# Performance work log

Measured on AMD Instinct MI355X. Metric: run time of the kernel, lower is better.

## Reference

```python
import jax, jax.numpy as jnp
from jax import lax
import numpy as np

GAMMA = 0.25        # inv_temp
C_SCALE = 1.0       # spectral_scale
STRIDE = 8          # patch stride (== patch_size, non-overlapping)


def setup_inputs() -> dict:
    key = jax.random.key(0)
    ks = jax.random.split(key, 9)
    B, C, H = 1024, 3, 64
    D, NP, M, NH, R, P = 256, 64, 1024, 8, 32, 8
    return {
        "x": jax.random.normal(ks[0], (B, C, H, H), jnp.float32),
        "z": jax.random.normal(ks[1], (B, NP, D), jnp.float32),
        "encoder_weight": jax.random.normal(ks[2], (D, C, P, P), jnp.float32) * 0.05,
        "encoder_bias": jax.random.normal(ks[3], (D,), jnp.float32) * 0.05,
        "visible_bias": jax.random.normal(ks[4], (C, H, H), jnp.float32) * 0.05,
        "pos_bias": jax.random.normal(ks[5], (NP, D), jnp.float32) * 0.05,
        "memory_weight": jax.random.normal(ks[6], (D, M), jnp.float32) * 0.05,
        "W_Q": jax.random.normal(ks[7], (NH, R, D), jnp.float32) * 0.05,
        "W_K": jax.random.normal(ks[8], (NH, R, D), jnp.float32) * 0.05,
    }


def reference(x, z, encoder_weight, encoder_bias, visible_bias, pos_bias,
              memory_weight, W_Q, W_K):
    """E = 0.5||x||^2 + 0.5||z||^2 - Phi_coupling(x, z); returns (B,)."""
    B = x.shape[0]
    D = encoder_weight.shape[0]

    quad_x = 0.5 * jnp.sum(x * x, axis=(1, 2, 3))
    quad_z = 0.5 * jnp.sum(z * z, axis=(1, 2))

    # visible-bias coupling
    phi_vis = jnp.sum(visible_bias[None] * x, axis=(1, 2, 3))

    # conv encode: (B, D, gh, gw) -> (B, NP, D)
    enc = lax.conv_general_dilated(
        x, C_SCALE * encoder_weight, window_strides=(STRIDE, STRIDE),
        padding='VALID', dimension_numbers=('NCHW', 'OIHW', 'NCHW'))
    encoded = enc.reshape(B, D, -1).transpose(0, 2, 1)  # (B, NP, D)

    # enc_act = 'none' -> identity
    phi_enc = jnp.sum(encoded * z, axis=(1, 2))
    phi_bias = jnp.sum(z * encoder_bias, axis=(1, 2))
    phi_pos = jnp.sum(z * pos_bias[None], axis=(1, 2))

    # memory ReLU^2 term: (B, NP, M)
    mem_proj = jnp.einsum('bpd,dm->bpm', z, C_SCALE * memory_weight)
    phi_mem = jnp.sum(jnp.square(jax.nn.relu(mem_proj)), axis=(1, 2))

    # Hopfield attention logsumexp term
    Q = jnp.einsum('bpd,hrd->bhrp', z, C_SCALE * W_Q)  # (B, H, R, NP)
    K = jnp.einsum('bpd,hrd->bhrp', z, C_SCALE * W_K)
    A = jnp.einsum('bhdm,bhdn->bhmn', Q, K)            # (B, H, NP, NP)
    phi_att = jnp.sum(jax.scipy.special.logsumexp(GAMMA * A, axis=-1),
                      axis=(1, 2)) / GAMMA

    coupling = phi_vis + phi_enc + phi_bias + phi_pos + phi_mem + phi_att
    return quad_x + quad_z - coupling
```

## Files before the change

### kernel.cpp

```cpp
#include <hip/hip_runtime.h>
#include <hip/hip_bf16.h>

#define GAMMA 0.25f


typedef __attribute__((ext_vector_type(8))) short short8;
typedef __attribute__((ext_vector_type(4))) float f32x4;

__device__ __forceinline__ float dot4(float4 a, float4 b) {
  return fmaf(a.x, b.x, fmaf(a.y, b.y, fmaf(a.z, b.z, a.w * b.w)));
}

__device__ __forceinline__ void fma4(float4& a, float s, float4 w) {
  a.x = fmaf(s, w.x, a.x); a.y = fmaf(s, w.y, a.y);
  a.z = fmaf(s, w.z, a.z); a.w = fmaf(s, w.w, a.w);
}

__device__ __forceinline__ ushort f2bf(float f) {
  __hip_bfloat16 h = __float2bfloat16(f);
  return *reinterpret_cast<ushort*>(&h);
}

__device__ __forceinline__ float bf2f(ushort u) {
  union { unsigned int i; float f; } v;
  v.i = ((unsigned int)u) << 16;
  return v.f;
}

__device__ __forceinline__ void bar_lds() {
  asm volatile("s_waitcnt lgkmcnt(0)" ::: "memory");
  __builtin_amdgcn_s_barrier();
  asm volatile("" ::: "memory");
}

__device__ __forceinline__ float block_sum_256(float v, float* tmp) {
#pragma unroll
  for (int off = 32; off; off >>= 1) v += __shfl_down(v, off, 64);
  int w = threadIdx.x >> 6;
  if ((threadIdx.x & 63) == 0) tmp[w] = v;
  __syncthreads();
  return tmp[0] + tmp[1] + tmp[2] + tmp[3];
}

__global__ __launch_bounds__(256) void k_z_cvt2(const float* __restrict__ z,
                                                const float* __restrict__ eb,
                                                const float* __restrict__ pb,
                                                float* __restrict__ out,
                                                ushort* __restrict__ zb16) {
  __shared__ float tmp[4];
  int bid = blockIdx.x, b = bid >> 1, hz = bid & 1, t = threadIdx.x;
  const float4* zb = (const float4*)(z + (size_t)b * 16384);
  const float4* pb4 = (const float4*)pb;
  const float4* eb4 = (const float4*)eb;
  ushort4* z16o = (ushort4*)(zb16 + (size_t)b * 16384);
  float s = 0.f;
  const int i0 = hz * 2048;
  for (int i = i0 + t; i < i0 + 2048; i += 256) {
    float4 zv = zb[i];
    float4 pv = pb4[i];
    float4 ev = eb4[i & 63];
    float4 c;
    c.x = pv.x + ev.x; c.y = pv.y + ev.y; c.z = pv.z + ev.z; c.w = pv.w + ev.w;
    s += 0.5f * dot4(zv, zv) - dot4(zv, c);
    ushort4 o;
    o.x = f2bf(zv.x); o.y = f2bf(zv.y); o.z = f2bf(zv.z); o.w = f2bf(zv.w);
    z16o[i] = o;
  }
  float r = block_sum_256(s, tmp);
  if (t == 0) atomicAdd(out + b, r);
}

__global__ __launch_bounds__(256) void k_cvt_weights_v3(
    const float* __restrict__ wq, const float* __restrict__ wk,
    const float* __restrict__ ew, const float* __restrict__ mw,
    ushort* __restrict__ wqf, ushort* __restrict__ wkf,
    ushort* __restrict__ ewt, ushort* __restrict__ mtf) {
  int bid = blockIdx.x, t = threadIdx.x;
  ushort o[8];
  if (bid < 64) {
    const float* src = (bid < 32) ? wq : wk;
    ushort* dst = (bid < 32) ? wqf : wkf;
    int tid = (bid & 31) * 256 + t;
    int frag = tid >> 6, l = tid & 63;
    int h = frag >> 4, nt = (frag >> 3) & 1, ks = frag & 7;
    const float* s = src + ((size_t)h * 32 + nt * 16 + (l & 15)) * 256 +
                     ks * 32 + (l >> 4) * 8;
#pragma unroll
    for (int i = 0; i < 8; ++i) o[i] = f2bf(s[i]);
    *(ushort4*)(dst + (size_t)tid * 8) = *(ushort4*)&o[0];
    *(ushort4*)(dst + (size_t)tid * 8 + 4) = *(ushort4*)&o[4];
  } else if (bid < 88) {
    int tid = (bid - 64) * 256 + t;
    int frag = tid >> 6, l = tid & 63;
    int ks = frag / 12, ct = frag % 12;
    const float* s = ew + (size_t)(ks * 32 + (l >> 4) * 8) * 192 +
                     ct * 16 + (l & 15);
#pragma unroll
    for (int i = 0; i < 8; ++i) o[i] = f2bf(s[(size_t)i * 192]);
    *(ushort4*)(ewt + (size_t)tid * 8) = *(ushort4*)&o[0];
    *(ushort4*)(ewt + (size_t)tid * 8 + 4) = *(ushort4*)&o[4];
  } else {
    int tid = (bid - 88) * 256 + t;
    int frag = tid >> 6, l = tid & 63;
    int C = frag >> 3, kc = frag & 7;
    int k0 = kc * 32 + (l >> 4) * 8, col = C * 16 + (l & 15);
#pragma unroll
    for (int i = 0; i < 8; ++i) o[i] = f2bf(mw[(size_t)(k0 + i) * 1024 + col]);
    *(ushort4*)(mtf + (size_t)tid * 8) = *(ushort4*)&o[0];
    *(ushort4*)(mtf + (size_t)tid * 8 + 4) = *(ushort4*)&o[4];
  }
}

__global__ __launch_bounds__(256) void k_enc_v3(
    const float* __restrict__ x, const float* __restrict__ vb,
    const ushort* __restrict__ ewt, const ushort* __restrict__ zb16,
    float* __restrict__ out) {
  __shared__ ushort xs[12288];
  __shared__ float tmp[4];
  const int b = blockIdx.x, t = threadIdx.x, l = t & 63, w = t >> 6;
  const int q = l >> 4, m = l & 15;

  const ushort* Az = zb16 + ((size_t)b * 64 + 16 * w + m) * 256 + q * 8;
  short8 a[8];
#pragma unroll
  for (int ks = 0; ks < 8; ++ks) a[ks] = *(const short8*)(Az + ks * 32);

  const float4* xb = (const float4*)(x + (size_t)b * 12288);
  const float4* vb4 = (const float4*)vb;
  ushort4* xs4 = (ushort4*)xs;
  float s = 0.f;
  for (int i = t; i < 3072; i += 256) {
    float4 xv = xb[i];
    float4 bv = vb4[i];
    s += 0.5f * dot4(xv, xv) - dot4(bv, xv);
    ushort4 o;
    o.x = f2bf(xv.x); o.y = f2bf(xv.y); o.z = f2bf(xv.z); o.w = f2bf(xv.w);
    xs4[i] = o;
  }
  __syncthreads();

  f32x4 acc[12];
#pragma unroll
  for (int ct = 0; ct < 12; ++ct) acc[ct] = f32x4{0.f, 0.f, 0.f, 0.f};

  const ushort* Ep = ewt + (size_t)l * 8;
  short8 fb[8];
#pragma unroll
  for (int i = 0; i < 8; ++i) fb[i] = *(const short8*)(Ep + i * 512);
#pragma unroll
  for (int f = 0; f < 96; ++f) {
    const int ks = f / 12, ct = f % 12;
    acc[ct] = __builtin_amdgcn_mfma_f32_16x16x32_bf16(a[ks], fb[f & 7],
                                                      acc[ct], 0, 0, 0);
    if (f < 88) fb[f & 7] = *(const short8*)(Ep + (size_t)(f + 8) * 512);
  }

#pragma unroll
  for (int ct = 0; ct < 12; ++ct) {
#pragma unroll
    for (int reg = 0; reg < 4; ++reg) {
      const int p = 16 * w + 4 * q + reg, gi = p >> 3, gj = p & 7;
      const int k = ct * 16 + m, c = k >> 6, r2 = k & 63;
      const int ii = r2 >> 3, jj = r2 & 7;
      s -= acc[ct][reg] * bf2f(xs[c * 4096 + (gi * 8 + ii) * 64 + gj * 8 + jj]);
    }
  }
  float r = block_sum_256(s, tmp);
  if (t == 0) atomicAdd(out + b, r);
}

__global__ __launch_bounds__(256) void k_mem_v5(const ushort* __restrict__ zb,
                                                const ushort* __restrict__ mtf,
                                                float* __restrict__ out) {
  __shared__ ushort zf[2048 * 8];
  __shared__ float tmp[4];
  const int t = threadIdx.x, l = t & 63, w = t >> 6;
  const int b = blockIdx.x >> 1, cth = blockIdx.x & 1;

#pragma unroll
  for (int j = 0; j < 8; ++j) {
    int i = t + j * 256;
    int l2 = i & 63, ks = (i >> 6) & 7, w2 = i >> 9;
    short8 v = *(const short8*)(zb + ((size_t)b * 64 + 16 * w2 + (l2 & 15)) * 256
                                + ks * 32 + (l2 >> 4) * 8);
    *(short8*)(zf + (size_t)i * 8) = v;
  }
  __syncthreads();

  float s = 0.f;
#pragma unroll 1
  for (int ctl = 0; ctl < 2; ++ctl) {
    const int ct = cth * 2 + ctl;
    const ushort* Bb = mtf + ((size_t)(ct * 16 + w * 4) * 8) * 512 + (size_t)l * 8;
    short8 fb[2][4];
#pragma unroll
    for (int c = 0; c < 4; ++c) fb[0][c] = *(const short8*)(Bb + (c * 8 + 0) * 512);
#pragma unroll
    for (int c = 0; c < 4; ++c) fb[1][c] = *(const short8*)(Bb + (c * 8 + 1) * 512);

    f32x4 acc[4][4];
#pragma unroll
    for (int r = 0; r < 4; ++r)
#pragma unroll
      for (int c = 0; c < 4; ++c) acc[r][c] = f32x4{0.f, 0.f, 0.f, 0.f};

#pragma unroll
    for (int kc = 0; kc < 8; ++kc) {
      const int cur = kc & 1;
      short8 a4[4];
#pragma unroll
      for (int r = 0; r < 4; ++r)
        a4[r] = *(const short8*)(zf + (size_t)((r * 8 + kc) * 64 + l) * 8);
#pragma unroll
      for (int r = 0; r < 4; ++r)
#pragma unroll
        for (int c = 0; c < 4; ++c)
          acc[r][c] = __builtin_amdgcn_mfma_f32_16x16x32_bf16(a4[r], fb[cur][c],
                                                              acc[r][c], 0, 0, 0);
      if (kc < 6) {
#pragma unroll
        for (int c = 0; c < 4; ++c)
          fb[cur][c] = *(const short8*)(Bb + (c * 8 + kc + 2) * 512);
      }
    }
#pragma unroll
    for (int r = 0; r < 4; ++r)
#pragma unroll
      for (int c = 0; c < 4; ++c)
#pragma unroll
        for (int e = 0; e < 4; ++e) {
          float rr = fmaxf(acc[r][c][e], 0.f);
          s = fmaf(rr, rr, s);
        }
  }
  float r = block_sum_256(s, tmp);
  if (t == 0) atomicAdd(out + b, -r);
}

__global__ __launch_bounds__(256) void k_attn_v5(
    const ushort* __restrict__ zb, const ushort* __restrict__ wqf,
    const ushort* __restrict__ wkf, float* __restrict__ out) {
  __shared__ ushort Qb[64 * 40];
  __shared__ ushort Kb[64 * 40];
  __shared__ float tmp[4];
  const int t = threadIdx.x, l = t & 63, w = t >> 6;
  const int b = blockIdx.x >> 1, half = blockIdx.x & 1;
  const int q = l >> 4, m = l & 15;

  const ushort* Az = zb + ((size_t)b * 64 + 16 * w + m) * 256 + q * 8;
  short8 a[8];
#pragma unroll
  for (int ks = 0; ks < 8; ++ks) a[ks] = *(const short8*)(Az + ks * 32);

  const ushort* Wq0 = wqf + (size_t)(half * 4) * 8192 + (size_t)l * 8;
  const ushort* Wk0 = wkf + (size_t)(half * 4) * 8192 + (size_t)l * 8;

  short8 fq0[3], fq1[3], fk0[3], fk1[3];
#pragma unroll
  for (int i = 0; i < 3; ++i) {
    fq0[i] = *(const short8*)(Wq0 + i * 512);
    fq1[i] = *(const short8*)(Wq0 + (8 + i) * 512);
    fk0[i] = *(const short8*)(Wk0 + i * 512);
    fk1[i] = *(const short8*)(Wk0 + (8 + i) * 512);
  }

  float part = 0.f;
#pragma unroll
  for (int hh = 0; hh < 4; ++hh) {
    f32x4 accq0 = f32x4{0.f, 0.f, 0.f, 0.f}, accq1 = accq0;
    f32x4 acck0 = accq0, acck1 = accq0;
#pragma unroll
    for (int ks = 0; ks < 8; ++ks) {
      const int gs = hh * 8 + ks, cur = gs % 3;
      accq0 = __builtin_amdgcn_mfma_f32_16x16x32_bf16(a[ks], fq0[cur], accq0, 0, 0, 0);
      accq1 = __builtin_amdgcn_mfma_f32_16x16x32_bf16(a[ks], fq1[cur], accq1, 0, 0, 0);
      acck0 = __builtin_amdgcn_mfma_f32_16x16x32_bf16(a[ks], fk0[cur], acck0, 0, 0, 0);
      acck1 = __builtin_amdgcn_mfma_f32_16x16x32_bf16(a[ks], fk1[cur], acck1, 0, 0, 0);
      const int gn = gs + 3;
      if (gn < 32) {
        const int hn = gn >> 3, ksn = gn & 7, sl = gn % 3;
        const ushort* Bqn = Wq0 + (size_t)hn * 8192;
        const ushort* Bkn = Wk0 + (size_t)hn * 8192;
        fq0[sl] = *(const short8*)(Bqn + ksn * 512);
        fq1[sl] = *(const short8*)(Bqn + (8 + ksn) * 512);
        fk0[sl] = *(const short8*)(Bkn + ksn * 512);
        fk1[sl] = *(const short8*)(Bkn + (8 + ksn) * 512);
      }
    }
    const int rowbase = (16 * w + 4 * q) * 40;
#pragma unroll
    for (int reg = 0; reg < 4; ++reg) {
      Qb[rowbase + reg * 40 + m]      = f2bf(accq0[reg]);
      Qb[rowbase + reg * 40 + 16 + m] = f2bf(accq1[reg]);
      Kb[rowbase + reg * 40 + m]      = f2bf(acck0[reg]);
      Kb[rowbase + reg * 40 + 16 + m] = f2bf(acck1[reg]);
    }
    bar_lds();

    short8 qa = *(const short8*)&Qb[(16 * w + m) * 40 + q * 8];
    f32x4 acc[4];
#pragma unroll
    for (int nt = 0; nt < 4; ++nt) {
      short8 kb = *(const short8*)&Kb[(16 * nt + m) * 40 + q * 8];
      acc[nt] = __builtin_amdgcn_mfma_f32_16x16x32_bf16(
          qa, kb, f32x4{0.f, 0.f, 0.f, 0.f}, 0, 0, 0);
    }
#pragma unroll
    for (int reg = 0; reg < 4; ++reg) {
      float e = __expf(GAMMA * acc[0][reg]) + __expf(GAMMA * acc[1][reg]) +
                __expf(GAMMA * acc[2][reg]) + __expf(GAMMA * acc[3][reg]);
      e += __shfl_xor(e, 1, 64);
      e += __shfl_xor(e, 2, 64);
      e += __shfl_xor(e, 4, 64);
      e += __shfl_xor(e, 8, 64);
      part += (m == 0) ? __logf(e) : 0.f;
    }
    bar_lds();
  }
  float tot = block_sum_256(part, tmp);
  if (t == 0) atomicAdd(out + b, -tot * (1.0f / GAMMA));
}

__global__ __launch_bounds__(256) void k_xz(const float* __restrict__ x,
                                            const float* __restrict__ z,
                                            const float* __restrict__ vb,
                                            const float* __restrict__ eb,
                                            const float* __restrict__ pb,
                                            float* __restrict__ out) {
  __shared__ float tmp[4];
  int b = blockIdx.x, t = threadIdx.x;
  const float4* xb = (const float4*)(x + (size_t)b * 12288);
  const float4* vb4 = (const float4*)vb;
  float s = 0.f;
  for (int i = t; i < 3072; i += 256) {
    float4 xv = xb[i];
    float4 bv = vb4[i];
    s += 0.5f * dot4(xv, xv) - dot4(bv, xv);
  }
  const float4* zb = (const float4*)(z + (size_t)b * 16384);
  const float4* pb4 = (const float4*)pb;
  const float4* eb4 = (const float4*)eb;
  for (int i = t; i < 4096; i += 256) {
    float4 zv = zb[i];
    float4 pv = pb4[i];
    float4 ev = eb4[i & 63];
    float4 c;
    c.x = pv.x + ev.x; c.y = pv.y + ev.y; c.z = pv.z + ev.z; c.w = pv.w + ev.w;
    s += 0.5f * dot4(zv, zv) - dot4(zv, c);
  }
  float r = block_sum_256(s, tmp);
  if (t == 0) out[b] = r;
}

__global__ __launch_bounds__(256) void k_enc(const float* __restrict__ x,
                                             const float* __restrict__ z,
                                             const float* __restrict__ ew,
                                             float* __restrict__ out) {
  __shared__ float xs[12288];
  __shared__ float tmp[4];
  int b = blockIdx.x, t = threadIdx.x;
  const float4* xb4 = (const float4*)(x + (size_t)b * 12288);
  for (int i = t; i < 3072; i += 256) ((float4*)xs)[i] = xb4[i];
  __syncthreads();

  float acc[64];
#pragma unroll
  for (int p = 0; p < 64; ++p) acc[p] = 0.f;

  for (int k4 = 0; k4 < 48; ++k4) {
    float4 wv = *(const float4*)(ew + (size_t)t * 192 + k4 * 4);
    int c = k4 >> 4;
    int ii = (k4 >> 1) & 7;
    int jh = (k4 & 1) * 4;
    const float* base = xs + c * 4096 + ii * 64 + jh;
#pragma unroll
    for (int p = 0; p < 64; ++p) {
      float4 pv = *(const float4*)(base + (p >> 3) * 512 + (p & 7) * 8);
      acc[p] = fmaf(wv.x, pv.x,
               fmaf(wv.y, pv.y, fmaf(wv.z, pv.z, fmaf(wv.w, pv.w, acc[p]))));
    }
  }
  const float* zb = z + (size_t)b * 16384;
  float s = 0.f;
#pragma unroll
  for (int p = 0; p < 64; ++p) s += acc[p] * zb[p * 256 + t];
  float r = block_sum_256(s, tmp);
  if (t == 0) atomicAdd(out + b, -r);
}

__global__ __launch_bounds__(256) void k_mem(const float* __restrict__ z,
                                             const float* __restrict__ mw,
                                             float* __restrict__ out) {
  __shared__ float zs[16 * 256];
  __shared__ float tmp[4];
  int b = blockIdx.x >> 2, pt = blockIdx.x & 3, t = threadIdx.x;
  const float4* zb4 = (const float4*)(z + (size_t)b * 16384 + pt * 4096);
  for (int i = t; i < 1024; i += 256) ((float4*)zs)[i] = zb4[i];
  __syncthreads();

  const float4* m4 = (const float4*)mw;
  float4 acc[16];
#pragma unroll
  for (int pp = 0; pp < 16; ++pp) acc[pp] = make_float4(0.f, 0.f, 0.f, 0.f);

#pragma unroll 2
  for (int k4 = 0; k4 < 64; ++k4) {
    float4 w0 = m4[(4 * k4 + 0) * 256 + t];
    float4 w1 = m4[(4 * k4 + 1) * 256 + t];
    float4 w2 = m4[(4 * k4 + 2) * 256 + t];
    float4 w3 = m4[(4 * k4 + 3) * 256 + t];
#pragma unroll
    for (int pp = 0; pp < 16; ++pp) {
      float4 zv = *(const float4*)&zs[pp * 256 + k4 * 4];
      fma4(acc[pp], zv.x, w0);
      fma4(acc[pp], zv.y, w1);
      fma4(acc[pp], zv.z, w2);
      fma4(acc[pp], zv.w, w3);
    }
  }
  float total = 0.f;
#pragma unroll
  for (int pp = 0; pp < 16; ++pp) {
    float r;
    r = fmaxf(acc[pp].x, 0.f); total = fmaf(r, r, total);
    r = fmaxf(acc[pp].y, 0.f); total = fmaf(r, r, total);
    r = fmaxf(acc[pp].z, 0.f); total = fmaf(r, r, total);
    r = fmaxf(acc[pp].w, 0.f); total = fmaf(r, r, total);
  }
  float r = block_sum_256(total, tmp);
  if (t == 0) atomicAdd(out + b, -r);
}

__global__ __launch_bounds__(256) void k_attn(const float* __restrict__ z,
                                              const float* __restrict__ wq,
                                              const float* __restrict__ wk,
                                              float* __restrict__ out) {
  __shared__ float lds[8192];
  __shared__ float red[4];
  const int b = blockIdx.x >> 1, half = blockIdx.x & 1;
  const int t = threadIdx.x;
  const int lane = t & 63;
  const int w = __builtin_amdgcn_readfirstlane(t >> 6);
  const float4* zb4 = (const float4*)(z + (size_t)b * 16384);

  float qa[4][8], ka[4][8];
#pragma unroll
  for (int hh = 0; hh < 4; ++hh)
#pragma unroll
    for (int j = 0; j < 8; ++j) { qa[hh][j] = 0.f; ka[hh][j] = 0.f; }

  float4* lds4 = (float4*)lds;
  for (int dc = 0; dc < 2; ++dc) {
    __syncthreads();
    for (int i = t; i < 2048; i += 256) {
      int p = i >> 5, ld4 = i & 31;
      lds4[ld4 * 64 + (p ^ (ld4 & 7))] = zb4[p * 64 + dc * 32 + ld4];
    }
    __syncthreads();
#pragma unroll
    for (int hh = 0; hh < 4; ++hh) {
      int h = half * 4 + hh;
      const float* Wqb = wq + (size_t)h * 8192 + (size_t)(w * 8) * 256 + dc * 128;
      const float* Wkb = wk + (size_t)h * 8192 + (size_t)(w * 8) * 256 + dc * 128;
      for (int ld4 = 0; ld4 < 32; ++ld4) {
        float4 wv[8], kv[8];
#pragma unroll
        for (int j = 0; j < 8; ++j) {
          wv[j] = *(const float4*)(Wqb + j * 256 + ld4 * 4);
          kv[j] = *(const float4*)(Wkb + j * 256 + ld4 * 4);
        }
        float4 zv = lds4[ld4 * 64 + (lane ^ (ld4 & 7))];
#pragma unroll
        for (int j = 0; j < 8; ++j) {
          qa[hh][j] = fmaf(wv[j].x, zv.x, fmaf(wv[j].y, zv.y,
                      fmaf(wv[j].z, zv.z, fmaf(wv[j].w, zv.w, qa[hh][j]))));
          ka[hh][j] = fmaf(kv[j].x, zv.x, fmaf(kv[j].y, zv.y,
                      fmaf(kv[j].z, zv.z, fmaf(kv[j].w, zv.w, ka[hh][j]))));
        }
      }
    }
  }

  float* Qs = lds;
  float* Ks = lds + 2048;
  float lse = 0.f;
#pragma unroll
  for (int hh = 0; hh < 4; ++hh) {
    __syncthreads();
#pragma unroll
    for (int j = 0; j < 8; ++j) {
      Qs[(w * 8 + j) * 64 + lane] = qa[hh][j];
      Ks[(w * 8 + j) * 64 + lane] = ka[hh][j];
    }
    __syncthreads();
    float av[16];
#pragma unroll
    for (int mm = 0; mm < 16; ++mm) av[mm] = 0.f;
    for (int rr = 0; rr < 32; ++rr) {
      float kv = Ks[rr * 64 + lane];
      const float* qrow = &Qs[rr * 64 + w * 16];
      float4 q0 = *(const float4*)(qrow + 0);
      float4 q1 = *(const float4*)(qrow + 4);
      float4 q2 = *(const float4*)(qrow + 8);
      float4 q3 = *(const float4*)(qrow + 12);
      av[0]  = fmaf(q0.x, kv, av[0]);  av[1]  = fmaf(q0.y, kv, av[1]);
      av[2]  = fmaf(q0.z, kv, av[2]);  av[3]  = fmaf(q0.w, kv, av[3]);
      av[4]  = fmaf(q1.x, kv, av[4]);  av[5]  = fmaf(q1.y, kv, av[5]);
      av[6]  = fmaf(q1.z, kv, av[6]);  av[7]  = fmaf(q1.w, kv, av[7]);
      av[8]  = fmaf(q2.x, kv, av[8]);  av[9]  = fmaf(q2.y, kv, av[9]);
      av[10] = fmaf(q2.z, kv, av[10]); av[11] = fmaf(q2.w, kv, av[11]);
      av[12] = fmaf(q3.x, kv, av[12]); av[13] = fmaf(q3.w, kv, av[13]);
      av[14] = fmaf(q3.z, kv, av[14]); av[15] = fmaf(q3.w, kv, av[15]);
    }
#pragma unroll
    for (int mm = 0; mm < 16; ++mm) {
      float e = __expf(GAMMA * av[mm]);
#pragma unroll
      for (int off = 32; off; off >>= 1) e += __shfl_xor(e, off, 64);
      lse += __logf(e);
    }
  }
  if (lane == 0) red[w] = lse;
  __syncthreads();
  if (t == 0)
    atomicAdd(out + b, -(red[0] + red[1] + red[2] + red[3]) * (1.0f / GAMMA));
}

extern "C" void kernel_launch(void* const* d_in, const int* in_sizes, int n_in,
                              void* d_out, int out_size, void* d_ws,
                              size_t ws_size, hipStream_t stream) {
  (void)in_sizes; (void)n_in; (void)out_size;
  const float* x  = (const float*)d_in[0];
  const float* z  = (const float*)d_in[1];
  const float* ew = (const float*)d_in[2];
  const float* eb = (const float*)d_in[3];
  const float* vb = (const float*)d_in[4];
  const float* pb = (const float*)d_in[5];
  const float* mw = (const float*)d_in[6];
  const float* wq = (const float*)d_in[7];
  const float* wk = (const float*)d_in[8];
  float* out = (float*)d_out;

  const size_t Z_B  = (size_t)1024 * 64 * 256 * 2;
  const size_t MT_B = (size_t)1024 * 256 * 2;
  const size_t W_B  = (size_t)8 * 32 * 256 * 2;
  const size_t EW_B = (size_t)96 * 64 * 8 * 2;
  const size_t FULL = Z_B + MT_B + 2 * W_B + EW_B;

  ushort* zb16 = (ushort*)d_ws;
  ushort* mtf  = (ushort*)((char*)d_ws + Z_B);
  ushort* wqf  = (ushort*)((char*)d_ws + Z_B + MT_B);
  ushort* wkf  = (ushort*)((char*)d_ws + Z_B + MT_B + W_B);
  ushort* ewt  = (ushort*)((char*)d_ws + Z_B + MT_B + 2 * W_B);

  if (ws_size >= FULL) {
    hipMemsetAsync(out, 0, 1024 * sizeof(float), stream);
    k_z_cvt2<<<2048, 256, 0, stream>>>(z, eb, pb, out, zb16);
    k_cvt_weights_v3<<<216, 256, 0, stream>>>(wq, wk, ew, mw,
                                              wqf, wkf, ewt, mtf);
    k_enc_v3 <<<1024, 256, 0, stream>>>(x, vb, ewt, zb16, out);
    k_mem_v5 <<<2048, 256, 0, stream>>>(zb16, mtf, out);
    k_attn_v5<<<2048, 256, 0, stream>>>(zb16, wqf, wkf, out);
  } else {
    k_xz  <<<1024, 256, 0, stream>>>(x, z, vb, eb, pb, out);
    k_enc <<<1024, 256, 0, stream>>>(x, z, ew, out);
    k_mem <<<4096, 256, 0, stream>>>(z, mw, out);
    k_attn<<<2048, 256, 0, stream>>>(z, wq, wk, out);
  }
}
```

Baseline: 261.2 us.

## Stage encoder weights in LDS and restructure attention projection as one tiled GEMM

The encoder kernel now stages each k-slice of the bf16 encoder weight into a double-buffered LDS tile shared by all four waves, replacing per-wave global fragment loads. The attention kernel concatenates W_Q and W_K into one interleaved weight so the QK projection becomes a single 64x256 GEMM. In that GEMM the z tile is staged in LDS and each wave computes a 4x4 block of MFMA tiles. Q/K results are then written to LDS once for all heads, which removes the per-head barriers. The costs are more LDS use and extra barriers in the encoder loop, and the fallback attention path also gets an index typo fixed (q3.w to q3.y).

```diff
diff --git a/kernel.cpp b/kernel.cpp
--- a/kernel.cpp
+++ b/kernel.cpp
@@ -25,12 +25,6 @@
   union { unsigned int i; float f; } v;
   v.i = ((unsigned int)u) << 16;
   return v.f;
-}
-
-__device__ __forceinline__ void bar_lds() {
-  asm volatile("s_waitcnt lgkmcnt(0)" ::: "memory");
-  __builtin_amdgcn_s_barrier();
-  asm volatile("" ::: "memory");
 }
 
 __device__ __forceinline__ float block_sum_256(float v, float* tmp) {
@@ -70,25 +64,25 @@
   if (t == 0) atomicAdd(out + b, r);
 }
 
-__global__ __launch_bounds__(256) void k_cvt_weights_v3(
+__global__ __launch_bounds__(256) void k_cvt_weights_v4(
     const float* __restrict__ wq, const float* __restrict__ wk,
     const float* __restrict__ ew, const float* __restrict__ mw,
-    ushort* __restrict__ wqf, ushort* __restrict__ wkf,
-    ushort* __restrict__ ewt, ushort* __restrict__ mtf) {
+    ushort* __restrict__ wcf, ushort* __restrict__ ewt,
+    ushort* __restrict__ mtf) {
   int bid = blockIdx.x, t = threadIdx.x;
   ushort o[8];
   if (bid < 64) {
-    const float* src = (bid < 32) ? wq : wk;
-    ushort* dst = (bid < 32) ? wqf : wkf;
-    int tid = (bid & 31) * 256 + t;
+    int tid = bid * 256 + t;
     int frag = tid >> 6, l = tid & 63;
-    int h = frag >> 4, nt = (frag >> 3) & 1, ks = frag & 7;
-    const float* s = src + ((size_t)h * 32 + nt * 16 + (l & 15)) * 256 +
-                     ks * 32 + (l >> 4) * 8;
+    int ctg = frag >> 3, kc = frag & 7;
+    int col = ctg * 16 + (l & 15);
+    int h = col >> 6, qk = (col >> 5) & 1, rr = col & 31;
+    int k0 = kc * 32 + (l >> 4) * 8;
+    const float* s = (qk ? wk : wq) + ((size_t)h * 32 + rr) * 256 + k0;
 #pragma unroll
     for (int i = 0; i < 8; ++i) o[i] = f2bf(s[i]);
-    *(ushort4*)(dst + (size_t)tid * 8) = *(ushort4*)&o[0];
-    *(ushort4*)(dst + (size_t)tid * 8 + 4) = *(ushort4*)&o[4];
+    *(ushort4*)(wcf + (size_t)tid * 8) = *(ushort4*)&o[0];
+    *(ushort4*)(wcf + (size_t)tid * 8 + 4) = *(ushort4*)&o[4];
   } else if (bid < 88) {
     int tid = (bid - 64) * 256 + t;
     int frag = tid >> 6, l = tid & 63;
@@ -111,11 +105,12 @@
   }
 }
 
-__global__ __launch_bounds__(256) void k_enc_v3(
+__global__ __launch_bounds__(256) void k_enc_v4(
     const float* __restrict__ x, const float* __restrict__ vb,
     const ushort* __restrict__ ewt, const ushort* __restrict__ zb16,
     float* __restrict__ out) {
   __shared__ ushort xs[12288];
+  __shared__ ushort ebuf[2][6144];
   __shared__ float tmp[4];
   const int b = blockIdx.x, t = threadIdx.x, l = t & 63, w = t >> 6;
   const int q = l >> 4, m = l & 15;
@@ -124,6 +119,11 @@
   short8 a[8];
 #pragma unroll
   for (int ks = 0; ks < 8; ++ks) a[ks] = *(const short8*)(Az + ks * 32);
+
+  short8 st[3];
+#pragma unroll
+  for (int i = 0; i < 3; ++i)
+    st[i] = *(const short8*)(ewt + (size_t)(t + i * 256) * 8);
 
   const float4* xb = (const float4*)(x + (size_t)b * 12288);
   const float4* vb4 = (const float4*)vb;
@@ -137,22 +137,35 @@
     o.x = f2bf(xv.x); o.y = f2bf(xv.y); o.z = f2bf(xv.z); o.w = f2bf(xv.w);
     xs4[i] = o;
   }
+#pragma unroll
+  for (int i = 0; i < 3; ++i)
+    *(short8*)(ebuf[0] + (size_t)(t + i * 256) * 8) = st[i];
   __syncthreads();
 
   f32x4 acc[12];
 #pragma unroll
   for (int ct = 0; ct < 12; ++ct) acc[ct] = f32x4{0.f, 0.f, 0.f, 0.f};
 
-  const ushort* Ep = ewt + (size_t)l * 8;
-  short8 fb[8];
-#pragma unroll
-  for (int i = 0; i < 8; ++i) fb[i] = *(const short8*)(Ep + i * 512);
-#pragma unroll
-  for (int f = 0; f < 96; ++f) {
-    const int ks = f / 12, ct = f % 12;
-    acc[ct] = __builtin_amdgcn_mfma_f32_16x16x32_bf16(a[ks], fb[f & 7],
-                                                      acc[ct], 0, 0, 0);
-    if (f < 88) fb[f & 7] = *(const short8*)(Ep + (size_t)(f + 8) * 512);
+#pragma unroll
+  for (int ks = 0; ks < 8; ++ks) {
+    const int cur = ks & 1;
+    if (ks < 7) {
+#pragma unroll
+      for (int i = 0; i < 3; ++i)
+        st[i] = *(const short8*)(ewt + (size_t)(ks + 1) * 6144 +
+                                 (size_t)(t + i * 256) * 8);
+    }
+#pragma unroll
+    for (int ct = 0; ct < 12; ++ct) {
+      short8 bv = *(const short8*)(ebuf[cur] + (size_t)(ct * 64 + l) * 8);
+      acc[ct] = __builtin_amdgcn_mfma_f32_16x16x32_bf16(a[ks], bv, acc[ct], 0, 0, 0);
+    }
+    if (ks < 7) {
+#pragma unroll
+      for (int i = 0; i < 3; ++i)
+        *(short8*)(ebuf[cur ^ 1] + (size_t)(t + i * 256) * 8) = st[i];
+    }
+    __syncthreads();
   }
 
 #pragma unroll
@@ -237,85 +250,94 @@
   if (t == 0) atomicAdd(out + b, -r);
 }
 
-__global__ __launch_bounds__(256) void k_attn_v5(
-    const ushort* __restrict__ zb, const ushort* __restrict__ wqf,
-    const ushort* __restrict__ wkf, float* __restrict__ out) {
-  __shared__ ushort Qb[64 * 40];
-  __shared__ ushort Kb[64 * 40];
+__global__ __launch_bounds__(256) void k_attn_v6(
+    const ushort* __restrict__ zb, const ushort* __restrict__ wcf,
+    float* __restrict__ out) {
+  __shared__ ushort ubuf[64 * 264];
   __shared__ float tmp[4];
   const int t = threadIdx.x, l = t & 63, w = t >> 6;
   const int b = blockIdx.x >> 1, half = blockIdx.x & 1;
   const int q = l >> 4, m = l & 15;
 
-  const ushort* Az = zb + ((size_t)b * 64 + 16 * w + m) * 256 + q * 8;
-  short8 a[8];
-#pragma unroll
-  for (int ks = 0; ks < 8; ++ks) a[ks] = *(const short8*)(Az + ks * 32);
-
-  const ushort* Wq0 = wqf + (size_t)(half * 4) * 8192 + (size_t)l * 8;
-  const ushort* Wk0 = wkf + (size_t)(half * 4) * 8192 + (size_t)l * 8;
-
-  short8 fq0[3], fq1[3], fk0[3], fk1[3];
-#pragma unroll
-  for (int i = 0; i < 3; ++i) {
-    fq0[i] = *(const short8*)(Wq0 + i * 512);
-    fq1[i] = *(const short8*)(Wq0 + (8 + i) * 512);
-    fk0[i] = *(const short8*)(Wk0 + i * 512);
-    fk1[i] = *(const short8*)(Wk0 + (8 + i) * 512);
-  }
+#pragma unroll
+  for (int j = 0; j < 8; ++j) {
+    int i = t + j * 256;
+    int l2 = i & 63, ks = (i >> 6) & 7, w2 = i >> 9;
+    short8 v = *(const short8*)(zb + ((size_t)b * 64 + 16 * w2 + (l2 & 15)) * 256
+                                + ks * 32 + (l2 >> 4) * 8);
+    *(short8*)(ubuf + (size_t)i * 8) = v;
+  }
+  __syncthreads();
+
+  const ushort* Bb = wcf + ((size_t)((half * 16 + w * 4) * 8)) * 512 +
+                     (size_t)l * 8;
+  short8 fb[2][4];
+#pragma unroll
+  for (int c = 0; c < 4; ++c) fb[0][c] = *(const short8*)(Bb + (c * 8 + 0) * 512);
+#pragma unroll
+  for (int c = 0; c < 4; ++c) fb[1][c] = *(const short8*)(Bb + (c * 8 + 1) * 512);
+
+  f32x4 acc[4][4];
+#pragma unroll
+  for (int r = 0; r < 4; ++r)
+#pragma unroll
+    for (int c = 0; c < 4; ++c) acc[r][c] = f32x4{0.f, 0.f, 0.f, 0.f};
+
+#pragma unroll
+  for (int kc = 0; kc < 8; ++kc) {
+    const int cur = kc & 1;
+    short8 a4[4];
+#pragma unroll
+    for (int r = 0; r < 4; ++r)
+      a4[r] = *(const short8*)(ubuf + (size_t)((r * 8 + kc) * 64 + l) * 8);
+#pragma unroll
+    for (int r = 0; r < 4; ++r)
+#pragma unroll
+      for (int c = 0; c < 4; ++c)
+        acc[r][c] = __builtin_amdgcn_mfma_f32_16x16x32_bf16(a4[r], fb[cur][c],
+                                                            acc[r][c], 0, 0, 0);
+    if (kc < 6) {
+#pragma unroll
+      for (int c = 0; c < 4; ++c)
+        fb[cur][c] = *(const short8*)(Bb + (c * 8 + kc + 2) * 512);
+    }
+  }
+  __syncthreads();
+
+  ushort* dstg = ubuf;
+#pragma unroll
+  for (int rt = 0; rt < 4; ++rt)
+#pragma unroll
+    for (int c = 0; c < 4; ++c)
+#pragma unroll
+      for (int reg = 0; reg < 4; ++reg)
+        dstg[(size_t)(16 * rt + 4 * q + reg) * 264 + (4 * w + c) * 16 + m] =
+            f2bf(acc[rt][c][reg]);
+  __syncthreads();
 
   float part = 0.f;
 #pragma unroll
   for (int hh = 0; hh < 4; ++hh) {
-    f32x4 accq0 = f32x4{0.f, 0.f, 0.f, 0.f}, accq1 = accq0;
-    f32x4 acck0 = accq0, acck1 = accq0;
-#pragma unroll
-    for (int ks = 0; ks < 8; ++ks) {
-      const int gs = hh * 8 + ks, cur = gs % 3;
-      accq0 = __builtin_amdgcn_mfma_f32_16x16x32_bf16(a[ks], fq0[cur], accq0, 0, 0, 0);
-      accq1 = __builtin_amdgcn_mfma_f32_16x16x32_bf16(a[ks], fq1[cur], accq1, 0, 0, 0);
-      acck0 = __builtin_amdgcn_mfma_f32_16x16x32_bf16(a[ks], fk0[cur], acck0, 0, 0, 0);
-      acck1 = __builtin_amdgcn_mfma_f32_16x16x32_bf16(a[ks], fk1[cur], acck1, 0, 0, 0);
-      const int gn = gs + 3;
-      if (gn < 32) {
-        const int hn = gn >> 3, ksn = gn & 7, sl = gn % 3;
-        const ushort* Bqn = Wq0 + (size_t)hn * 8192;
-        const ushort* Bkn = Wk0 + (size_t)hn * 8192;
-        fq0[sl] = *(const short8*)(Bqn + ksn * 512);
-        fq1[sl] = *(const short8*)(Bqn + (8 + ksn) * 512);
-        fk0[sl] = *(const short8*)(Bkn + ksn * 512);
-        fk1[sl] = *(const short8*)(Bkn + (8 + ksn) * 512);
-      }
-    }
-    const int rowbase = (16 * w + 4 * q) * 40;
+    short8 qa = *(const short8*)(dstg + (size_t)(16 * w + m) * 264 +
+                                 hh * 64 + q * 8);
+    f32x4 a2[4];
+#pragma unroll
+    for (int nt = 0; nt < 4; ++nt) {
+      short8 kb = *(const short8*)(dstg + (size_t)(16 * nt + m) * 264 +
+                                   hh * 64 + 32 + q * 8);
+      a2[nt] = __builtin_amdgcn_mfma_f32_16x16x32_bf16(
+          qa, kb, f32x4{0.f, 0.f, 0.f, 0.f}, 0, 0, 0);
+    }
 #pragma unroll
     for (int reg = 0; reg < 4; ++reg) {
-      Qb[rowbase + reg * 40 + m]      = f2bf(accq0[reg]);
-      Qb[rowbase + reg * 40 + 16 + m] = f2bf(accq1[reg]);
-      Kb[rowbase + reg * 40 + m]      = f2bf(acck0[reg]);
-      Kb[rowbase + reg * 40 + 16 + m] = f2bf(acck1[reg]);
-    }
-    bar_lds();
-
-    short8 qa = *(const short8*)&Qb[(16 * w + m) * 40 + q * 8];
-    f32x4 acc[4];
-#pragma unroll
-    for (int nt = 0; nt < 4; ++nt) {
-      short8 kb = *(const short8*)&Kb[(16 * nt + m) * 40 + q * 8];
-      acc[nt] = __builtin_amdgcn_mfma_f32_16x16x32_bf16(
-          qa, kb, f32x4{0.f, 0.f, 0.f, 0.f}, 0, 0, 0);
-    }
-#pragma unroll
-    for (int reg = 0; reg < 4; ++reg) {
-      float e = __expf(GAMMA * acc[0][reg]) + __expf(GAMMA * acc[1][reg]) +
-                __expf(GAMMA * acc[2][reg]) + __expf(GAMMA * acc[3][reg]);
+      float e = __expf(GAMMA * a2[0][reg]) + __expf(GAMMA * a2[1][reg]) +
+                __expf(GAMMA * a2[2][reg]) + __expf(GAMMA * a2[3][reg]);
       e += __shfl_xor(e, 1, 64);
       e += __shfl_xor(e, 2, 64);
       e += __shfl_xor(e, 4, 64);
       e += __shfl_xor(e, 8, 64);
       part += (m == 0) ? __logf(e) : 0.f;
     }
-    bar_lds();
   }
   float tot = block_sum_256(part, tmp);
   if (t == 0) atomicAdd(out + b, -tot * (1.0f / GAMMA));
@@ -509,7 +531,7 @@
       av[6]  = fmaf(q1.z, kv, av[6]);  av[7]  = fmaf(q1.w, kv, av[7]);
       av[8]  = fmaf(q2.x, kv, av[8]);  av[9]  = fmaf(q2.y, kv, av[9]);
       av[10] = fmaf(q2.z, kv, av[10]); av[11] = fmaf(q2.w, kv, av[11]);
-      av[12] = fmaf(q3.x, kv, av[12]); av[13] = fmaf(q3.w, kv, av[13]);
+      av[12] = fmaf(q3.x, kv, av[12]); av[13] = fmaf(q3.y, kv, av[13]);
       av[14] = fmaf(q3.z, kv, av[14]); av[15] = fmaf(q3.w, kv, av[15]);
     }
 #pragma unroll
@@ -543,24 +565,22 @@
 
   const size_t Z_B  = (size_t)1024 * 64 * 256 * 2;
   const size_t MT_B = (size_t)1024 * 256 * 2;
-  const size_t W_B  = (size_t)8 * 32 * 256 * 2;
   const size_t EW_B = (size_t)96 * 64 * 8 * 2;
-  const size_t FULL = Z_B + MT_B + 2 * W_B + EW_B;
+  const size_t WC_B = (size_t)512 * 256 * 2;
+  const size_t FULL = Z_B + MT_B + EW_B + WC_B;
 
   ushort* zb16 = (ushort*)d_ws;
   ushort* mtf  = (ushort*)((char*)d_ws + Z_B);
-  ushort* wqf  = (ushort*)((char*)d_ws + Z_B + MT_B);
-  ushort* wkf  = (ushort*)((char*)d_ws + Z_B + MT_B + W_B);
-  ushort* ewt  = (ushort*)((char*)d_ws + Z_B + MT_B + 2 * W_B);
+  ushort* ewt  = (ushort*)((char*)d_ws + Z_B + MT_B);
+  ushort* wcf  = (ushort*)((char*)d_ws + Z_B + MT_B + EW_B);
 
   if (ws_size >= FULL) {
     hipMemsetAsync(out, 0, 1024 * sizeof(float), stream);
     k_z_cvt2<<<2048, 256, 0, stream>>>(z, eb, pb, out, zb16);
-    k_cvt_weights_v3<<<216, 256, 0, stream>>>(wq, wk, ew, mw,
-                                              wqf, wkf, ewt, mtf);
-    k_enc_v3 <<<1024, 256, 0, stream>>>(x, vb, ewt, zb16, out);
+    k_cvt_weights_v4<<<216, 256, 0, stream>>>(wq, wk, ew, mw, wcf, ewt, mtf);
+    k_enc_v4 <<<1024, 256, 0, stream>>>(x, vb, ewt, zb16, out);
     k_mem_v5 <<<2048, 256, 0, stream>>>(zb16, mtf, out);
-    k_attn_v5<<<2048, 256, 0, stream>>>(zb16, wqf, wkf, out);
+    k_attn_v6<<<2048, 256, 0, stream>>>(zb16, wcf, out);
   } else {
     k_xz  <<<1024, 256, 0, stream>>>(x, z, vb, eb, pb, out);
     k_enc <<<1024, 256, 0, stream>>>(x, z, ew, out);
```

Measured after the change: 253.9 us. 1.03x faster.
